# Performance work log

Hardware: AMD Instinct MI355X
Metric: run time of the kernel (lower is better)

The kernel has to match this reference:

```python
import jax, jax.numpy as jnp
import numpy as np

BATCH = 16384
NUM_CLASSES = 1024  # power of 2 -> exact complete binary NBDT hierarchy, depth 10


def setup_inputs() -> dict:
    key = jax.random.key(0)
    outputs = jax.random.normal(key, (BATCH, NUM_CLASSES), dtype=jnp.float32)
    return {"outputs": outputs}


def reference(outputs) -> jnp.ndarray:
    """SoftEmbeddedDecisionRules.forward over a complete balanced binary tree.

    For every internal node: node_logits[child] = mean of outputs over the
    leaf classes under that child (get_node_logits), probs = softmax over
    children (get_all_node_outputs), and class_probs[:, leaves_under_child]
    *= probs[:, child] (traverse_tree). With a balanced binary tree, nodes at
    depth d split classes into 2^d blocks of 2 equal halves, so each level
    vectorizes into one reshape/mean/softmax/multiply.
    """
    B, C = outputs.shape
    depth = int(np.log2(C))
    class_probs = jnp.ones((B, C), dtype=outputs.dtype)
    for d in range(depth):
        n_nodes = 1 << d            # nodes at this tree level
        blk = C // (2 * n_nodes)    # leaves per child
        # gather-mean: node logits [B, n_nodes, 2]
        node_logits = outputs.reshape(B, n_nodes, 2, blk).mean(axis=-1)
        probs = jax.nn.softmax(node_logits, axis=-1)  # per-node softmax over children
        # scatter-multiply into class probabilities
        class_probs = (class_probs.reshape(B, n_nodes, 2, blk)
                       * probs[..., None]).reshape(B, C)
    return class_probs
```

## Files before the change

kernel.cpp:

```cpp
#include <hip/hip_runtime.h>

#define NBDT_BATCH 16384
#define NBDT_C 1024

__device__ __forceinline__ float fast_sigmoid(float x) {
    return __builtin_amdgcn_rcpf(1.0f + __expf(-x));
}

__global__ __launch_bounds__(256) void nbdt_kernel(const float* __restrict__ x,
                                                   float* __restrict__ y) {
    const int wave = (blockIdx.x * 256 + threadIdx.x) >> 6;
    const int lane = threadIdx.x & 63;
    const size_t rowbase = (size_t)wave * NBDT_C + (size_t)lane * 4;

    float e[4][4];
#pragma unroll
    for (int k = 0; k < 4; ++k) {
        float4 v = *reinterpret_cast<const float4*>(x + rowbase + k * 256);
        e[k][0] = v.x; e[k][1] = v.y; e[k][2] = v.z; e[k][3] = v.w;
    }

    float s2[4][2], s4[4], s256[4];
    float d4[4], d8[4], d16[4], d32[4], d64[4], d128[4];
#pragma unroll
    for (int k = 0; k < 4; ++k) {
        s2[k][0] = e[k][0] + e[k][1];
        s2[k][1] = e[k][2] + e[k][3];
        s4[k] = s2[k][0] + s2[k][1];
        float acc = s4[k];
        float t;
        t = __shfl_xor(acc, 1);  d4[k]   = acc - t;  acc += t;
        t = __shfl_xor(acc, 2);  d8[k]   = acc - t;  acc += t;
        t = __shfl_xor(acc, 4);  d16[k]  = acc - t;  acc += t;
        t = __shfl_xor(acc, 8);  d32[k]  = acc - t;  acc += t;
        t = __shfl_xor(acc, 16); d64[k]  = acc - t;  acc += t;
        t = __shfl_xor(acc, 32); d128[k] = acc - t;  acc += t;
        s256[k] = acc;
    }

    const float S512a = s256[0] + s256[1];
    const float S512b = s256[2] + s256[3];
    const float pTop = fast_sigmoid((S512a - S512b) * (1.0f / 512.0f));
    const float qTop = 1.0f - pTop;
    const float p01  = fast_sigmoid((s256[0] - s256[1]) * (1.0f / 256.0f));
    const float p23  = fast_sigmoid((s256[2] - s256[3]) * (1.0f / 256.0f));
    float P[4];
    P[0] = pTop * p01;  P[1] = pTop - P[0];
    P[2] = qTop * p23;  P[3] = qTop - P[2];

#pragma unroll
    for (int k = 0; k < 4; ++k) {
        float Pk = P[k];
        Pk *= fast_sigmoid(d128[k] * (1.0f / 128.0f));
        Pk *= fast_sigmoid(d64[k]  * (1.0f / 64.0f));
        Pk *= fast_sigmoid(d32[k]  * (1.0f / 32.0f));
        Pk *= fast_sigmoid(d16[k]  * (1.0f / 16.0f));
        Pk *= fast_sigmoid(d8[k]   * (1.0f / 8.0f));
        Pk *= fast_sigmoid(d4[k]   * (1.0f / 4.0f));

        float c0 = Pk * fast_sigmoid((s2[k][0] - s2[k][1]) * 0.5f);
        float c1 = Pk - c0;
        float4 o;
        o.x = c0 * fast_sigmoid(e[k][0] - e[k][1]);
        o.y = c0 - o.x;
        o.z = c1 * fast_sigmoid(e[k][2] - e[k][3]);
        o.w = c1 - o.z;
        *reinterpret_cast<float4*>(y + rowbase + k * 256) = o;
    }
}

extern "C" void kernel_launch(void* const* d_in, const int* in_sizes, int n_in,
                              void* d_out, int out_size, void* d_ws, size_t ws_size,
                              hipStream_t stream) {
    const float* x = (const float*)d_in[0];
    float* y = (float*)d_out;
    dim3 grid(NBDT_BATCH / 4);
    dim3 block(256);
    nbdt_kernel<<<grid, block, 0, stream>>>(x, y);
}
```

Baseline: 107.7 us.

## Give each lane 8 contiguous elements and fold sigmoid chain into one reciprocal

Each lane now owns 8 contiguous classes in two 512-wide halves instead of 4 contiguous classes in four 256-wide quarters. This cuts the shuffle reduction chains from four to two per lane. The product of sigmoids along the root-to-leaf path is rewritten as a single reciprocal of a product of (1+exp) terms, which removes per-level rcp instructions. In exchange the loads become two float4 per 512-block, which may reduce coalescing per instruction, and multiplying the (1+exp) terms together risks overflow when logit differences are large.

Measured after the change: 112.0 us. 4.0% more time.

```diff
diff --git a/kernel.cpp b/kernel.cpp
--- a/kernel.cpp
+++ b/kernel.cpp
@@ -11,61 +11,66 @@
                                                    float* __restrict__ y) {
     const int wave = (blockIdx.x * 256 + threadIdx.x) >> 6;
     const int lane = threadIdx.x & 63;
-    const size_t rowbase = (size_t)wave * NBDT_C + (size_t)lane * 4;
+    const size_t rowbase = (size_t)wave * NBDT_C + (size_t)lane * 8;
+    const float* xp = x + rowbase;
+    float* yp = y + rowbase;
 
-    float e[4][4];
+    float4 v[2][2];
 #pragma unroll
-    for (int k = 0; k < 4; ++k) {
-        float4 v = *reinterpret_cast<const float4*>(x + rowbase + k * 256);
-        e[k][0] = v.x; e[k][1] = v.y; e[k][2] = v.z; e[k][3] = v.w;
+    for (int k = 0; k < 2; ++k) {
+        v[k][0] = *reinterpret_cast<const float4*>(xp + k * 512);
+        v[k][1] = *reinterpret_cast<const float4*>(xp + k * 512 + 4);
     }
 
-    float s2[4][2], s4[4], s256[4];
-    float d4[4], d8[4], d16[4], d32[4], d64[4], d128[4];
+    float s4[2][2], d[2][6], s512[2];
 #pragma unroll
-    for (int k = 0; k < 4; ++k) {
-        s2[k][0] = e[k][0] + e[k][1];
-        s2[k][1] = e[k][2] + e[k][3];
-        s4[k] = s2[k][0] + s2[k][1];
-        float acc = s4[k];
+    for (int k = 0; k < 2; ++k) {
+        s4[k][0] = (v[k][0].x + v[k][0].y) + (v[k][0].z + v[k][0].w);
+        s4[k][1] = (v[k][1].x + v[k][1].y) + (v[k][1].z + v[k][1].w);
+        float acc = s4[k][0] + s4[k][1];
         float t;
-        t = __shfl_xor(acc, 1);  d4[k]   = acc - t;  acc += t;
-        t = __shfl_xor(acc, 2);  d8[k]   = acc - t;  acc += t;
-        t = __shfl_xor(acc, 4);  d16[k]  = acc - t;  acc += t;
-        t = __shfl_xor(acc, 8);  d32[k]  = acc - t;  acc += t;
-        t = __shfl_xor(acc, 16); d64[k]  = acc - t;  acc += t;
-        t = __shfl_xor(acc, 32); d128[k] = acc - t;  acc += t;
-        s256[k] = acc;
+        t = __shfl_xor(acc, 1);  d[k][0] = acc - t; acc += t;
+        t = __shfl_xor(acc, 2);  d[k][1] = acc - t; acc += t;
+        t = __shfl_xor(acc, 4);  d[k][2] = acc - t; acc += t;
+        t = __shfl_xor(acc, 8);  d[k][3] = acc - t; acc += t;
+        t = __shfl_xor(acc, 16); d[k][4] = acc - t; acc += t;
+        t = __shfl_xor(acc, 32); d[k][5] = acc - t; acc += t;
+        s512[k] = acc;
     }
 
-    const float S512a = s256[0] + s256[1];
-    const float S512b = s256[2] + s256[3];
-    const float pTop = fast_sigmoid((S512a - S512b) * (1.0f / 512.0f));
-    const float qTop = 1.0f - pTop;
-    const float p01  = fast_sigmoid((s256[0] - s256[1]) * (1.0f / 256.0f));
-    const float p23  = fast_sigmoid((s256[2] - s256[3]) * (1.0f / 256.0f));
-    float P[4];
-    P[0] = pTop * p01;  P[1] = pTop - P[0];
-    P[2] = qTop * p23;  P[3] = qTop - P[2];
+    const float xr = (s512[0] - s512[1]) * (1.0f / 512.0f);
+    const float eR[2] = { __expf(-xr), __expf(xr) };
 
 #pragma unroll
-    for (int k = 0; k < 4; ++k) {
-        float Pk = P[k];
-        Pk *= fast_sigmoid(d128[k] * (1.0f / 128.0f));
-        Pk *= fast_sigmoid(d64[k]  * (1.0f / 64.0f));
-        Pk *= fast_sigmoid(d32[k]  * (1.0f / 32.0f));
-        Pk *= fast_sigmoid(d16[k]  * (1.0f / 16.0f));
-        Pk *= fast_sigmoid(d8[k]   * (1.0f / 8.0f));
-        Pk *= fast_sigmoid(d4[k]   * (1.0f / 4.0f));
+    for (int k = 0; k < 2; ++k) {
+        float q = 1.0f + eR[k];
+        q *= 1.0f + __expf(d[k][5] * (-1.0f / 256.0f));
+        q *= 1.0f + __expf(d[k][4] * (-1.0f / 128.0f));
+        q *= 1.0f + __expf(d[k][3] * (-1.0f / 64.0f));
+        q *= 1.0f + __expf(d[k][2] * (-1.0f / 32.0f));
+        q *= 1.0f + __expf(d[k][1] * (-1.0f / 16.0f));
+        q *= 1.0f + __expf(d[k][0] * (-1.0f / 8.0f));
+        const float P = __builtin_amdgcn_rcpf(q);
 
-        float c0 = Pk * fast_sigmoid((s2[k][0] - s2[k][1]) * 0.5f);
-        float c1 = Pk - c0;
-        float4 o;
-        o.x = c0 * fast_sigmoid(e[k][0] - e[k][1]);
-        o.y = c0 - o.x;
-        o.z = c1 * fast_sigmoid(e[k][2] - e[k][3]);
-        o.w = c1 - o.z;
-        *reinterpret_cast<float4*>(y + rowbase + k * 256) = o;
+        float c0 = P * fast_sigmoid((s4[k][0] - s4[k][1]) * 0.25f);
+        float c1 = P - c0;
+
+        float4 a = v[k][0];
+        float4 b = v[k][1];
+        float4 o0, o1;
+
+        float e0 = c0 * fast_sigmoid(((a.x + a.y) - (a.z + a.w)) * 0.5f);
+        float e1 = c0 - e0;
+        o0.x = e0 * fast_sigmoid(a.x - a.y);  o0.y = e0 - o0.x;
+        o0.z = e1 * fast_sigmoid(a.z - a.w);  o0.w = e1 - o0.z;
+
+        float f0 = c1 * fast_sigmoid(((b.x + b.y) - (b.z + b.w)) * 0.5f);
+        float f1 = c1 - f0;
+        o1.x = f0 * fast_sigmoid(b.x - b.y);  o1.y = f0 - o1.x;
+        o1.z = f1 * fast_sigmoid(b.z - b.w);  o1.w = f1 - o1.z;
+
+        *reinterpret_cast<float4*>(yp + k * 512)     = o0;
+        *reinterpret_cast<float4*>(yp + k * 512 + 4) = o1;
     }
 }
 
```
